# Kernel optimization log

Hardware: AMD Instinct MI355X
Metric: run time of the kernel (lower is better)

Reference implementation:

```python
import jax, jax.numpy as jnp
import numpy as np

D_MODEL = 192
D_STATE = 16
D_CONV = 4
EXPAND = 2
D_INNER = EXPAND * D_MODEL
DT_RANK = (D_MODEL + 15) // 16  # ceil(d_model/16) = 12


def setup_inputs() -> dict:
    key = jax.random.key(0)
    ks = jax.random.split(key, 12)
    B, C, H, W = 16, D_MODEL, 64, 64
    s = lambda n: 0.02
    return {
        "x": jax.random.normal(ks[0], (B, C, H, W), jnp.float32),
        "ln_g": jnp.ones((C,), jnp.float32),
        "ln_b": jnp.zeros((C,), jnp.float32),
        "W_in": jax.random.normal(ks[1], (D_MODEL, 2 * D_INNER), jnp.float32) * s(0),
        "conv_w": jax.random.normal(ks[2], (D_INNER, D_CONV), jnp.float32) * 0.1,
        "conv_b": jnp.zeros((D_INNER,), jnp.float32),
        "W_x": jax.random.normal(ks[3], (D_INNER, DT_RANK + 2 * D_STATE), jnp.float32) * s(0),
        "W_dt": jax.random.normal(ks[4], (DT_RANK, D_INNER), jnp.float32) * 0.1,
        "b_dt": jax.random.uniform(ks[5], (D_INNER,), jnp.float32, -4.0, -1.0),
        "A_log": jnp.log(jnp.broadcast_to(jnp.arange(1, D_STATE + 1, dtype=jnp.float32), (D_INNER, D_STATE))),
        "Dp": jnp.ones((D_INNER,), jnp.float32),
        "W_out": jax.random.normal(ks[6], (D_INNER, D_MODEL), jnp.float32) * s(0),
    }


def _layernorm2d(x, g, b, eps=1e-5):
    # x: (B, C, H, W); normalize over channel dim
    mu = jnp.mean(x, axis=1, keepdims=True)
    var = jnp.var(x, axis=1, keepdims=True)
    xn = (x - mu) * jax.lax.rsqrt(var + eps)
    return xn * g[None, :, None, None] + b[None, :, None, None]


def _mamba(x, W_in, conv_w, conv_b, W_x, W_dt, b_dt, A_log, Dp, W_out):
    # x: (B, L, d_model)
    B, L, _ = x.shape
    xz = x @ W_in                       # (B, L, 2*d_inner)
    xi, z = jnp.split(xz, 2, axis=-1)   # each (B, L, d_inner)

    # causal depthwise conv over L
    xc = jnp.transpose(xi, (0, 2, 1))   # (B, d_inner, L)
    k = conv_w[:, None, :]              # (d_inner, 1, d_conv)
    xc = jax.lax.conv_general_dilated(
        xc, k, window_strides=(1,), padding=[(D_CONV - 1, 0)],
        dimension_numbers=("NCH", "OIH", "NCH"), feature_group_count=D_INNER)
    xc = xc + conv_b[None, :, None]
    u = jax.nn.silu(jnp.transpose(xc, (0, 2, 1)))  # (B, L, d_inner)

    xdbc = u @ W_x                      # (B, L, dt_rank + 2*d_state)
    dt_r, Bm, Cm = jnp.split(xdbc, [DT_RANK, DT_RANK + D_STATE], axis=-1)
    dt = jax.nn.softplus(dt_r @ W_dt + b_dt)  # (B, L, d_inner)
    A = -jnp.exp(A_log)                 # (d_inner, d_state)

    def step(h, inp):
        u_t, dt_t, B_t, C_t = inp       # (B,di), (B,di), (B,ds), (B,ds)
        dA = jnp.exp(dt_t[..., None] * A)              # (B, di, ds)
        dBu = (dt_t * u_t)[..., None] * B_t[:, None, :]  # (B, di, ds)
        h = h * dA + dBu
        y = jnp.einsum("bds,bs->bd", h, C_t)
        return h, y

    h0 = jnp.zeros((B, D_INNER, D_STATE), x.dtype)
    seq = (jnp.moveaxis(u, 1, 0), jnp.moveaxis(dt, 1, 0),
           jnp.moveaxis(Bm, 1, 0), jnp.moveaxis(Cm, 1, 0))
    _, ys = jax.lax.scan(step, h0, seq)
    y = jnp.moveaxis(ys, 0, 1) + u * Dp  # (B, L, d_inner)
    y = y * jax.nn.silu(z)
    return y @ W_out                    # (B, L, d_model)


def reference(x, ln_g, ln_b, W_in, conv_w, conv_b, W_x, W_dt, b_dt, A_log, Dp, W_out):
    b, c, h, w = x.shape
    residual = x
    xn = _layernorm2d(x, ln_g, ln_b)
    seq = jnp.transpose(xn.reshape(b, c, h * w), (0, 2, 1))  # (B, L, C)
    out = _mamba(seq, W_in, conv_w, conv_b, W_x, W_dt, b_dt, A_log, Dp, W_out)
    out = jnp.transpose(out, (0, 2, 1)).reshape(b, c, h, w)
    return out + residual
```

## Files before the change

### kernel.cpp

```cpp
#include <hip/hip_runtime.h>

typedef unsigned short u16;
typedef unsigned int u32;
typedef __attribute__((ext_vector_type(8))) short short8;
typedef __attribute__((ext_vector_type(4))) float f32x4;
typedef __attribute__((ext_vector_type(2))) float f32x2;

#define DEV __device__ __forceinline__

DEV float b2f(u16 u) { union { u32 i; float f; } v; v.i = ((u32)u) << 16; return v.f; }
DEV u16 f2b(float f) {
  union { float f; u32 i; } v; v.f = f;
  u32 r = v.i + 0x7FFFu + ((v.i >> 16) & 1u);
  return (u16)(r >> 16);
}
DEV bool sniff_f32(const void* ln_g) { return ((const u32*)ln_g)[0] == 0x3F800000u; }
DEV float rdv(const void* p, size_t i, bool f32) {
  return f32 ? ((const float*)p)[i] : b2f(((const u16*)p)[i]);
}

__global__ __launch_bounds__(256) void k0_prep(
    const void* __restrict__ W_in, const void* __restrict__ W_out,
    const void* __restrict__ W_x, const void* __restrict__ W_dt,
    const void* __restrict__ b_dt, const void* __restrict__ conv_w,
    const void* __restrict__ conv_b, const void* __restrict__ A_log,
    const void* __restrict__ Dp, const void* __restrict__ ln_g,
    const void* __restrict__ ln_b,
    u16* __restrict__ WinT, u16* __restrict__ WoutT, u16* __restrict__ WbigT,
    float* __restrict__ BdtF, float* __restrict__ convW, float* __restrict__ convB,
    float* __restrict__ AlnF, float* __restrict__ DpF,
    float* __restrict__ lnG, float* __restrict__ lnB) {
  const bool f32 = sniff_f32(ln_g);
  int i = blockIdx.x * 256 + threadIdx.x;
  if (i < 147456) { int n = i / 192, k = i - n * 192; WinT[i] = f2b(rdv(W_in, (size_t)k * 768 + n, f32)); return; }
  i -= 147456;
  if (i < 73728) { int c = i / 384, d = i - c * 384; WoutT[i] = f2b(rdv(W_out, (size_t)d * 192 + c, f32)); return; }
  i -= 73728;
  if (i < 196608) {
    int n = i / 384, k = i - n * 384;
    float v;
    if (n < 384) {
      v = 0.f;
      for (int r = 0; r < 12; ++r)
        v = fmaf(rdv(W_x, (size_t)k * 44 + r, f32), rdv(W_dt, (size_t)r * 384 + n, f32), v);
    } else if (n < 400) {
      v = rdv(W_x, (size_t)k * 44 + 12 + (n - 384), f32);
    } else if (n < 416) {
      v = rdv(W_x, (size_t)k * 44 + 28 + (n - 400), f32);
    } else {
      v = 0.f;
    }
    WbigT[i] = f2b(v);
    return;
  }
  i -= 196608;
  if (i < 384) { BdtF[i] = rdv(b_dt, i, f32); return; }
  i -= 384;
  if (i < 1536) { convW[i] = rdv(conv_w, i, f32); return; }
  i -= 1536;
  if (i < 384) { convB[i] = rdv(conv_b, i, f32); return; }
  i -= 384;
  if (i < 6144) { AlnF[i] = -__expf(rdv(A_log, i, f32)); return; }
  i -= 6144;
  if (i < 384) { DpF[i] = rdv(Dp, i, f32); return; }
  i -= 384;
  if (i < 192) { lnG[i] = rdv(ln_g, i, f32); return; }
  i -= 192;
  if (i < 192) { lnB[i] = rdv(ln_b, i, f32); return; }
}

__global__ __launch_bounds__(192) void k1_ln(
    const void* __restrict__ xg, const void* __restrict__ lng_raw,
    const float* __restrict__ lnG, const float* __restrict__ lnB,
    u16* __restrict__ xn) {
  const bool f32 = sniff_f32(lng_raw);
  const int b = blockIdx.y, l0 = blockIdx.x * 64, t = threadIdx.x;
  __shared__ float xs[192][65];
  __shared__ float rs[3][64], rq[3][64], smu[64], srstd[64];

  for (int i = t; i < 192 * 64; i += 192) {
    int c = i >> 6, l = i & 63;
    xs[c][l] = rdv(xg, ((size_t)(b * 192 + c)) * 4096 + l0 + l, f32);
  }
  __syncthreads();
  const int part = t >> 6, l = t & 63;
  float s = 0.f, q2 = 0.f;
  for (int cc = 0; cc < 64; ++cc) {
    float v = xs[part * 64 + cc][l];
    s += v; q2 = fmaf(v, v, q2);
  }
  rs[part][l] = s; rq[part][l] = q2;
  __syncthreads();
  if (t < 64) {
    float S = rs[0][t] + rs[1][t] + rs[2][t];
    float Q = rq[0][t] + rq[1][t] + rq[2][t];
    float mu = S * (1.0f / 192.0f);
    float var = Q * (1.0f / 192.0f) - mu * mu;
    smu[t] = mu; srstd[t] = rsqrtf(var + 1e-5f);
  }
  __syncthreads();
  const float gv = lnG[t], bv = lnB[t];
  for (int ll = 0; ll < 64; ++ll) {
    float v = (xs[t][ll] - smu[ll]) * srstd[ll];
    xn[((size_t)(b * 4096 + l0 + ll)) * 192 + t] = f2b(fmaf(v, gv, bv));
  }
}

__global__ __launch_bounds__(256) void k2_gemm1(
    const u16* __restrict__ WinT, const u16* __restrict__ xn,
    u16* __restrict__ xz) {
  const int ch0 = blockIdx.x * 128, l0 = blockIdx.y * 128, b = blockIdx.z;
  const int tid = threadIdx.x;
  const int wave = tid >> 6, lane = tid & 63;
  const int wr = wave >> 1, wc = wave & 1;
  const int q = lane >> 4, lm = lane & 15;

  __shared__ __align__(16) u16 As[128][72];
  __shared__ __align__(16) u16 Bs[128][72];

  f32x4 acc[4][4];
#pragma unroll
  for (int i = 0; i < 4; ++i)
#pragma unroll
    for (int j = 0; j < 4; ++j) acc[i][j] = (f32x4){0.f, 0.f, 0.f, 0.f};

  const int r4 = tid >> 3, c8 = (tid & 7) * 8;

  for (int kb = 0; kb < 3; ++kb) {
    const int c0 = kb * 64;
    __syncthreads();
#pragma unroll
    for (int p = 0; p < 4; ++p) {
      int r = p * 32 + r4;
      *(uint4*)&As[r][c8] = *(const uint4*)(WinT + (size_t)(ch0 + r) * 192 + c0 + c8);
      *(uint4*)&Bs[r][c8] = *(const uint4*)(xn + ((size_t)b * 4096 + l0 + r) * 192 + c0 + c8);
    }
    __syncthreads();
#pragma unroll
    for (int ks = 0; ks < 2; ++ks) {
      short8 a[4], bfr[4];
#pragma unroll
      for (int mt = 0; mt < 4; ++mt)
        a[mt] = *(const short8*)&As[wr * 64 + mt * 16 + lm][ks * 32 + q * 8];
#pragma unroll
      for (int nt = 0; nt < 4; ++nt)
        bfr[nt] = *(const short8*)&Bs[wc * 64 + nt * 16 + lm][ks * 32 + q * 8];
#pragma unroll
      for (int mt = 0; mt < 4; ++mt)
#pragma unroll
        for (int nt = 0; nt < 4; ++nt)
          acc[mt][nt] = __builtin_amdgcn_mfma_f32_16x16x32_bf16(a[mt], bfr[nt], acc[mt][nt], 0, 0, 0);
    }
  }
#pragma unroll
  for (int mt = 0; mt < 4; ++mt)
#pragma unroll
    for (int nt = 0; nt < 4; ++nt) {
      int n = l0 + wc * 64 + nt * 16 + lm;
#pragma unroll
      for (int reg = 0; reg < 4; ++reg) {
        int m = ch0 + wr * 64 + mt * 16 + q * 4 + reg;
        xz[((size_t)b * 768 + m) * 4096 + n] = f2b(acc[mt][nt][reg]);
      }
    }
}

__global__ __launch_bounds__(256) void k3_conv(
    u16* __restrict__ xz, const float* __restrict__ convW,
    const float* __restrict__ convB) {
  const int d = blockIdx.x, b = blockIdx.y, t = threadIdx.x;
  u16* row = xz + ((size_t)b * 768 + d) * 4096;
  __shared__ __align__(16) u16 srow[4096];
#pragma unroll
  for (int p = 0; p < 2; ++p)
    *(uint4*)&srow[p * 2048 + t * 8] = *(const uint4*)(row + p * 2048 + t * 8);
  __syncthreads();
  const float w0 = convW[d * 4 + 0], w1 = convW[d * 4 + 1];
  const float w2 = convW[d * 4 + 2], w3 = convW[d * 4 + 3];
  const float cb = convB[d];
  const int l = t * 16;
  u16 o[16];
#pragma unroll
  for (int i = 0; i < 16; ++i) {
    int li = l + i;
    float x0 = (li >= 3) ? b2f(srow[li - 3]) : 0.f;
    float x1 = (li >= 2) ? b2f(srow[li - 2]) : 0.f;
    float x2 = (li >= 1) ? b2f(srow[li - 1]) : 0.f;
    float x3 = b2f(srow[li]);
    float s = w0 * x0 + w1 * x1 + w2 * x2 + w3 * x3 + cb;
    float sig = 1.0f / (1.0f + __expf(-s));
    o[i] = f2b(s * sig);
  }
#pragma unroll
  for (int i = 0; i < 4; ++i) {
    ushort4 st; st.x = o[i * 4 + 0]; st.y = o[i * 4 + 1];
    st.z = o[i * 4 + 2]; st.w = o[i * 4 + 3];
    *(ushort4*)(row + l + i * 4) = st;
  }
}

__global__ __launch_bounds__(256) void k4_mfma(
    const u16* __restrict__ WbigT, const u16* __restrict__ xz,
    const float* __restrict__ BdtF,
    u16* __restrict__ dtb, float* __restrict__ Btl, float* __restrict__ Ctl) {
  const int ch0 = blockIdx.x * 128, l0 = blockIdx.y * 128, b = blockIdx.z;
  const int tid = threadIdx.x;
  const int wave = tid >> 6, lane = tid & 63;
  const int wr = wave >> 1, wc = wave & 1;
  const int q = lane >> 4, lm = lane & 15;

  __shared__ __align__(16) u16 As[128][72];
  __shared__ __align__(16) u16 Bs[128][72];

  f32x4 acc[4][4];
#pragma unroll
  for (int i = 0; i < 4; ++i)
#pragma unroll
    for (int j = 0; j < 4; ++j) acc[i][j] = (f32x4){0.f, 0.f, 0.f, 0.f};

  const int r4 = tid >> 3, c8 = (tid & 7) * 8;
  const int rb = tid >> 5, l4b = (tid & 31) * 4;

  for (int kb = 0; kb < 6; ++kb) {
    const int d0 = kb * 64;
    __syncthreads();
#pragma unroll
    for (int p = 0; p < 4; ++p) {
      int r = p * 32 + r4;
      *(uint4*)&As[r][c8] = *(const uint4*)(WbigT + (size_t)(ch0 + r) * 384 + d0 + c8);
    }
#pragma unroll
    for (int p = 0; p < 8; ++p) {
      int dd = p * 8 + rb;
      ushort4 vv = *(const ushort4*)(xz + ((size_t)b * 768 + d0 + dd) * 4096 + l0 + l4b);
      const int g = dd >> 3, d7 = dd & 7;
      const u16 vals[4] = {vv.x, vv.y, vv.z, vv.w};
#pragma unroll
      for (int i = 0; i < 4; ++i) {
        int l = l4b + i;
        int sc = (((g ^ ((l >> 2) & 7)) << 3) | d7);
        Bs[l][sc] = vals[i];
      }
    }
    __syncthreads();
#pragma unroll
    for (int ks = 0; ks < 2; ++ks) {
      short8 a[4], bfr[4];
#pragma unroll
      for (int mt = 0; mt < 4; ++mt)
        a[mt] = *(const short8*)&As[wr * 64 + mt * 16 + lm][ks * 32 + q * 8];
#pragma unroll
      for (int nt = 0; nt < 4; ++nt) {
        int row = wc * 64 + nt * 16 + lm;
        int g2 = (ks * 4 + q) ^ ((row >> 2) & 7);
        bfr[nt] = *(const short8*)&Bs[row][g2 * 8];
      }
#pragma unroll
      for (int mt = 0; mt < 4; ++mt)
#pragma unroll
        for (int nt = 0; nt < 4; ++nt)
          acc[mt][nt] = __builtin_amdgcn_mfma_f32_16x16x32_bf16(a[mt], bfr[nt], acc[mt][nt], 0, 0, 0);
    }
  }
#pragma unroll
  for (int mt = 0; mt < 4; ++mt) {
    const int tbase = ch0 + wr * 64 + mt * 16;
#pragma unroll
    for (int nt = 0; nt < 4; ++nt) {
      const int l = l0 + wc * 64 + nt * 16 + lm;
      if (tbase < 384) {
#pragma unroll
        for (int reg = 0; reg < 4; ++reg) {
          int m = tbase + q * 4 + reg;
          float v = acc[mt][nt][reg] + BdtF[m];
          float sp = __logf(1.0f + __expf(v));
          dtb[((size_t)b * 384 + m) * 4096 + l] = f2b(sp);
        }
      } else if (tbase == 384) {
        float4 v; v.x = acc[mt][nt][0]; v.y = acc[mt][nt][1];
        v.z = acc[mt][nt][2]; v.w = acc[mt][nt][3];
        *(float4*)(Btl + (((size_t)b * 4096 + l) << 4) + q * 4) = v;
      } else if (tbase == 400) {
        float4 v; v.x = acc[mt][nt][0]; v.y = acc[mt][nt][1];
        v.z = acc[mt][nt][2]; v.w = acc[mt][nt][3];
        *(float4*)(Ctl + (((size_t)b * 4096 + l) << 4) + q * 4) = v;
      }
    }
  }
}

#define NCH 128
#define TCH 32

DEV void build_e8p(float dt, const float* ap, int sbase, bool powok, f32x2* e2) {
  if (powok) {
    float q1 = __expf(-dt);
    float q2 = q1 * q1, q3 = q2 * q1, q4 = q2 * q2;
    float q5 = q4 * q1, q6 = q4 * q2, q7 = q4 * q3, q8 = q4 * q4;
    f32x2 m2; m2.x = sbase ? q8 : 1.0f; m2.y = m2.x;
    f32x2 a0; a0.x = q1; a0.y = q2;
    f32x2 a1; a1.x = q3; a1.y = q4;
    f32x2 a2; a2.x = q5; a2.y = q6;
    f32x2 a3; a3.x = q7; a3.y = q8;
    e2[0] = a0 * m2; e2[1] = a1 * m2; e2[2] = a2 * m2; e2[3] = a3 * m2;
  } else {
#pragma unroll
    for (int k = 0; k < 4; ++k) {
      f32x2 v;
      v.x = __expf(dt * ap[sbase + 2 * k]);
      v.y = __expf(dt * ap[sbase + 2 * k + 1]);
      e2[k] = v;
    }
  }
}

__global__ __launch_bounds__(64) void k5a_part(
    const u16* __restrict__ dtg, const u16* __restrict__ xz,
    const float* __restrict__ Btl, const float* __restrict__ AlnF,
    u16* __restrict__ Sbuf, float* __restrict__ sumdt) {
  const int cx = blockIdx.x, dg0 = blockIdx.y * 32, b = blockIdx.z;
  const int t = threadIdx.x;
  const int sh = t >> 5, dl = t & 31;
  const int sbase = sh * 8;
  const int lc = cx * TCH;
  __shared__ __align__(16) u16 sdt[32][40], su[32][40];
  __shared__ __align__(16) float sB[TCH][16];
#pragma unroll
  for (int i = t; i < 128; i += 64) {
    int r = i >> 2, c8 = (i & 3) * 8;
    *(uint4*)&sdt[r][c8] = *(const uint4*)(dtg + ((size_t)b * 384 + dg0 + r) * 4096 + lc + c8);
    *(uint4*)&su[r][c8] = *(const uint4*)(xz + ((size_t)b * 768 + dg0 + r) * 4096 + lc + c8);
  }
#pragma unroll
  for (int i = t; i < 128; i += 64) {
    int r = i >> 2, c4 = (i & 3) * 4;
    *(float4*)&sB[r][c4] = *(const float4*)(Btl + (((size_t)b * 4096 + lc + r) << 4) + c4);
  }
  __syncthreads();

  const float* ap = AlnF + (dg0 + dl) * 16;
  bool powok = true;
#pragma unroll
  for (int k = 0; k < 8; ++k)
    powok = powok && (fabsf(ap[sbase + k] + (float)(sbase + k + 1)) < 1e-3f * (float)(sbase + k + 1));

  f32x2 S2[4];
#pragma unroll
  for (int k = 0; k < 4; ++k) S2[k] = (f32x2){0.f, 0.f};
  float sdsum = 0.f;

#pragma unroll 1
  for (int l8 = 0; l8 < TCH / 8; ++l8) {
    short8 d8 = *(const short8*)&sdt[dl][l8 * 8];
    short8 u8 = *(const short8*)&su[dl][l8 * 8];
#pragma unroll
    for (int j = 0; j < 8; ++j) {
      float dt = b2f((u16)d8[j]);
      float uu = b2f((u16)u8[j]);
      float dtu = dt * uu;
      sdsum += dt;
      f32x2 e2[4];
      build_e8p(dt, ap, sbase, powok, e2);
      const float* Bp = &sB[l8 * 8 + j][sbase];
      float4 Bv0 = *(const float4*)(Bp);
      float4 Bv1 = *(const float4*)(Bp + 4);
      f32x2 dtu2; dtu2.x = dtu; dtu2.y = dtu;
      f32x2 b0; b0.x = Bv0.x; b0.y = Bv0.y;
      f32x2 b1; b1.x = Bv0.z; b1.y = Bv0.w;
      f32x2 b2; b2.x = Bv1.x; b2.y = Bv1.y;
      f32x2 b3; b3.x = Bv1.z; b3.y = Bv1.w;
      S2[0] = S2[0] * e2[0] + dtu2 * b0;
      S2[1] = S2[1] * e2[1] + dtu2 * b1;
      S2[2] = S2[2] * e2[2] + dtu2 * b2;
      S2[3] = S2[3] * e2[3] + dtu2 * b3;
    }
  }
  const size_t base = (((size_t)b * NCH + cx) * 384 + dg0 + dl) * 16 + sbase;
  u32 w[4];
#pragma unroll
  for (int k = 0; k < 4; ++k)
    w[k] = (u32)f2b(S2[k].x) | ((u32)f2b(S2[k].y) << 16);
  uint4 st0; st0.x = w[0]; st0.y = w[1]; st0.z = w[2]; st0.w = w[3];
  *(uint4*)(Sbuf + base) = st0;
  if (sh == 0)
    sumdt[((size_t)b * NCH + cx) * 384 + dg0 + dl] = sdsum;
}

__global__ __launch_bounds__(256) void k5b_comb(
    u16* __restrict__ Sbuf, const float* __restrict__ sumdt,
    const float* __restrict__ AlnF) {
  const int idx = blockIdx.x * 256 + threadIdx.x;
  const int s = idx & 15;
  const int bd = idx >> 4;
  const int d = bd % 384;
  const float a = AlnF[d * 16 + s];
  const size_t base0 = (size_t)bd * 16 + s;
  const float* sdp = sumdt + bd;
  float h = 0.f;
  float Sv_next = b2f(Sbuf[base0]);
  float sd_next = sdp[0];
  for (int c = 0; c < NCH; ++c) {
    float Sv = Sv_next, sd = sd_next;
    if (c + 1 < NCH) {
      Sv_next = b2f(Sbuf[base0 + (size_t)(c + 1) * 6144]);
      sd_next = sdp[(size_t)(c + 1) * 384];
    }
    Sbuf[base0 + (size_t)c * 6144] = f2b(h);
    h = fmaf(h, __expf(a * sd), Sv);
  }
}

__global__ __launch_bounds__(64) void k5c_scan(
    const u16* __restrict__ dtg, u16* __restrict__ xz,
    const float* __restrict__ Btl, const float* __restrict__ Ctl,
    const u16* __restrict__ Sbuf, const float* __restrict__ AlnF,
    const float* __restrict__ DpF) {
  const int cx = blockIdx.x, dg0 = blockIdx.y * 32, b = blockIdx.z;
  const int t = threadIdx.x;
  const int sh = t >> 5, dl = t & 31;
  const int sbase = sh * 8;
  const int lc = cx * TCH;
  __shared__ __align__(16) u16 sdt[32][40], su[32][40], sz[32][40];
  __shared__ __align__(16) float sB[TCH][16], sC[TCH][16];
#pragma unroll
  for (int i = t; i < 128; i += 64) {
    int r = i >> 2, c8 = (i & 3) * 8;
    *(uint4*)&sdt[r][c8] = *(const uint4*)(dtg + ((size_t)b * 384 + dg0 + r) * 4096 + lc + c8);
    *(uint4*)&su[r][c8] = *(const uint4*)(xz + ((size_t)b * 768 + dg0 + r) * 4096 + lc + c8);
    *(uint4*)&sz[r][c8] = *(const uint4*)(xz + ((size_t)b * 768 + 384 + dg0 + r) * 4096 + lc + c8);
  }
#pragma unroll
  for (int i = t; i < 128; i += 64) {
    int r = i >> 2, c4 = (i & 3) * 4;
    *(float4*)&sB[r][c4] = *(const float4*)(Btl + (((size_t)b * 4096 + lc + r) << 4) + c4);
    *(float4*)&sC[r][c4] = *(const float4*)(Ctl + (((size_t)b * 4096 + lc + r) << 4) + c4);
  }
  __syncthreads();

  const float* ap = AlnF + (dg0 + dl) * 16;
  bool powok = true;
#pragma unroll
  for (int k = 0; k < 8; ++k)
    powok = powok && (fabsf(ap[sbase + k] + (float)(sbase + k + 1)) < 1e-3f * (float)(sbase + k + 1));
  const float Dpl = DpF[dg0 + dl];

  f32x2 h2[4];
  {
    const size_t base = (((size_t)b * NCH + cx) * 384 + dg0 + dl) * 16 + sbase;
    uint4 s0 = *(const uint4*)(Sbuf + base);
    const u32 w[4] = {s0.x, s0.y, s0.z, s0.w};
#pragma unroll
    for (int k = 0; k < 4; ++k) {
      f32x2 v; v.x = b2f((u16)(w[k] & 0xFFFF)); v.y = b2f((u16)(w[k] >> 16));
      h2[k] = v;
    }
  }

  u16* zrow = xz + ((size_t)b * 768 + 384 + dg0 + dl) * 4096;

#pragma unroll 1
  for (int l8 = 0; l8 < TCH / 8; ++l8) {
    short8 d8 = *(const short8*)&sdt[dl][l8 * 8];
    short8 u8 = *(const short8*)&su[dl][l8 * 8];
    short8 z8 = *(const short8*)&sz[dl][l8 * 8];
    float yh[8];
#pragma unroll
    for (int j = 0; j < 8; ++j) {
      float dt = b2f((u16)d8[j]);
      float uu = b2f((u16)u8[j]);
      float dtu = dt * uu;
      f32x2 e2[4];
      build_e8p(dt, ap, sbase, powok, e2);
      const float* Bp = &sB[l8 * 8 + j][sbase];
      const float* Cp = &sC[l8 * 8 + j][sbase];
      float4 Bv0 = *(const float4*)(Bp);
      float4 Bv1 = *(const float4*)(Bp + 4);
      float4 Cv0 = *(const float4*)(Cp);
      float4 Cv1 = *(const float4*)(Cp + 4);
      f32x2 dtu2; dtu2.x = dtu; dtu2.y = dtu;
      f32x2 b0; b0.x = Bv0.x; b0.y = Bv0.y;
      f32x2 b1; b1.x = Bv0.z; b1.y = Bv0.w;
      f32x2 b2; b2.x = Bv1.x; b2.y = Bv1.y;
      f32x2 b3; b3.x = Bv1.z; b3.y = Bv1.w;
      f32x2 c0; c0.x = Cv0.x; c0.y = Cv0.y;
      f32x2 c1; c1.x = Cv0.z; c1.y = Cv0.w;
      f32x2 c2; c2.x = Cv1.x; c2.y = Cv1.y;
      f32x2 c3; c3.x = Cv1.z; c3.y = Cv1.w;
      h2[0] = h2[0] * e2[0] + dtu2 * b0;
      h2[1] = h2[1] * e2[1] + dtu2 * b1;
      h2[2] = h2[2] * e2[2] + dtu2 * b2;
      h2[3] = h2[3] * e2[3] + dtu2 * b3;
      f32x2 y2 = h2[0] * c0;
      y2 = h2[1] * c1 + y2;
      y2 = h2[2] * c2 + y2;
      y2 = h2[3] * c3 + y2;
      yh[j] = y2.x + y2.y;
    }
    u32 ya[4];
#pragma unroll
    for (int j = 0; j < 8; ++j) {
      float yfull = yh[j] + __shfl_xor(yh[j], 32, 64);
      float uu2 = b2f((u16)u8[j]);
      float zz2 = b2f((u16)z8[j]);
      float yf = fmaf(uu2, Dpl, yfull);
      float sig = 1.0f / (1.0f + __expf(-zz2));
      yf *= zz2 * sig;
      u16 yb = f2b(yf);
      if (j & 1) ya[j >> 1] |= ((u32)yb << 16);
      else ya[j >> 1] = (u32)yb;
    }
    if (sh == 0) {
      uint4 st; st.x = ya[0]; st.y = ya[1]; st.z = ya[2]; st.w = ya[3];
      *(uint4*)(zrow + lc + l8 * 8) = st;
    }
  }
}

__global__ __launch_bounds__(256) void k6_gemm2(
    const u16* __restrict__ WoutT, const u16* __restrict__ xz,
    const void* __restrict__ xg, const void* __restrict__ lng_raw,
    void* __restrict__ outg) {
  const bool f32 = sniff_f32(lng_raw);
  const int l0 = blockIdx.x * 128, b = blockIdx.y;
  const int tid = threadIdx.x;
  const int wave = tid >> 6, lane = tid & 63;
  const int wm = wave >> 1, wn = wave & 1;
  const int q = lane >> 4, lm = lane & 15;

  __shared__ __align__(16) u16 As[192][72];
  __shared__ __align__(16) u16 Bs[128][72];

  f32x4 acc[6][4];
#pragma unroll
  for (int i = 0; i < 6; ++i)
#pragma unroll
    for (int j = 0; j < 4; ++j) acc[i][j] = (f32x4){0.f, 0.f, 0.f, 0.f};

  const int ra = tid >> 3, c8 = (tid & 7) * 8;
  const int rb = tid >> 5, l4b = (tid & 31) * 4;

  for (int kb = 0; kb < 6; ++kb) {
    const int d0 = kb * 64;
    __syncthreads();
#pragma unroll
    for (int p = 0; p < 6; ++p) {
      int r = p * 32 + ra;
      *(uint4*)&As[r][c8] = *(const uint4*)(WoutT + (size_t)r * 384 + d0 + c8);
    }
#pragma unroll
    for (int p = 0; p < 8; ++p) {
      int dd = p * 8 + rb;
      ushort4 vv = *(const ushort4*)(xz + ((size_t)b * 768 + 384 + d0 + dd) * 4096 + l0 + l4b);
      const int g = dd >> 3, d7 = dd & 7;
      const u16 vals[4] = {vv.x, vv.y, vv.z, vv.w};
#pragma unroll
      for (int i = 0; i < 4; ++i) {
        int l = l4b + i;
        int sc = (((g ^ ((l >> 2) & 7)) << 3) | d7);
        Bs[l][sc] = vals[i];
      }
    }
    __syncthreads();
#pragma unroll
    for (int ks = 0; ks < 2; ++ks) {
      short8 a[6], bfr[4];
#pragma unroll
      for (int mt = 0; mt < 6; ++mt)
        a[mt] = *(const short8*)&As[wm * 96 + mt * 16 + lm][ks * 32 + q * 8];
#pragma unroll
      for (int nt = 0; nt < 4; ++nt) {
        int row = wn * 64 + nt * 16 + lm;
        int g2 = (ks * 4 + q) ^ ((row >> 2) & 7);
        bfr[nt] = *(const short8*)&Bs[row][g2 * 8];
      }
#pragma unroll
      for (int mt = 0; mt < 6; ++mt)
#pragma unroll
        for (int nt = 0; nt < 4; ++nt)
          acc[mt][nt] = __builtin_amdgcn_mfma_f32_16x16x32_bf16(a[mt], bfr[nt], acc[mt][nt], 0, 0, 0);
    }
  }
  if (f32) {
    float* op = (float*)outg;
    const float* xp = (const float*)xg;
#pragma unroll
    for (int mt = 0; mt < 6; ++mt)
#pragma unroll
      for (int nt = 0; nt < 4; ++nt) {
        int l = l0 + wn * 64 + nt * 16 + lm;
#pragma unroll
        for (int reg = 0; reg < 4; ++reg) {
          int m = wm * 96 + mt * 16 + q * 4 + reg;
          size_t idx = ((size_t)b * 192 + m) * 4096 + l;
          op[idx] = acc[mt][nt][reg] + xp[idx];
        }
      }
  } else {
    u16* op = (u16*)outg;
    const u16* xp = (const u16*)xg;
#pragma unroll
    for (int mt = 0; mt < 6; ++mt)
#pragma unroll
      for (int nt = 0; nt < 4; ++nt) {
        int l = l0 + wn * 64 + nt * 16 + lm;
#pragma unroll
        for (int reg = 0; reg < 4; ++reg) {
          int m = wm * 96 + mt * 16 + q * 4 + reg;
          size_t idx = ((size_t)b * 192 + m) * 4096 + l;
          op[idx] = f2b(acc[mt][nt][reg] + b2f(xp[idx]));
        }
      }
  }
}

extern "C" void kernel_launch(void* const* d_in, const int* in_sizes, int n_in,
                              void* d_out, int out_size, void* d_ws, size_t ws_size,
                              hipStream_t stream) {
  (void)in_sizes; (void)n_in; (void)out_size; (void)ws_size;
  const void* x      = d_in[0];
  const void* ln_g   = d_in[1];
  const void* ln_b   = d_in[2];
  const void* W_in   = d_in[3];
  const void* conv_w = d_in[4];
  const void* conv_b = d_in[5];
  const void* W_x    = d_in[6];
  const void* W_dt   = d_in[7];
  const void* b_dt   = d_in[8];
  const void* A_log  = d_in[9];
  const void* Dp     = d_in[10];
  const void* W_out  = d_in[11];

  char* ws = (char*)d_ws;
  u16*   xz    = (u16*)(ws + 0);
  u16*   xn    = (u16*)(ws + 100663296);
  u16*   dtb   = (u16*)(ws + 100663296);
  float* Btl   = (float*)(ws + 150994944);
  float* Ctl   = (float*)(ws + 155189248);
  u16*   Sbuf  = (u16*)(ws + 159383552);
  float* sumdt = (float*)(ws + 184549376);
  u16*   WinT  = (u16*)(ws + 187695104);
  u16*   WoutT = (u16*)(ws + 187990016);
  u16*   WbigT = (u16*)(ws + 188137472);
  float* BdtF  = (float*)(ws + 188530688);
  float* convW = (float*)(ws + 188532224);
  float* convB = (float*)(ws + 188538368);
  float* AlnF  = (float*)(ws + 188539904);
  float* DpF   = (float*)(ws + 188564480);
  float* lnG   = (float*)(ws + 188566016);
  float* lnB   = (float*)(ws + 188566784);

  k0_prep<<<dim3(1668), dim3(256), 0, stream>>>(
      W_in, W_out, W_x, W_dt, b_dt, conv_w, conv_b, A_log, Dp, ln_g, ln_b,
      WinT, WoutT, WbigT, BdtF, convW, convB, AlnF, DpF, lnG, lnB);
  k1_ln<<<dim3(64, 16), dim3(192), 0, stream>>>(x, ln_g, lnG, lnB, xn);
  k2_gemm1<<<dim3(6, 32, 16), dim3(256), 0, stream>>>(WinT, xn, xz);
  k3_conv<<<dim3(384, 16), dim3(256), 0, stream>>>(xz, convW, convB);
  k4_mfma<<<dim3(4, 32, 16), dim3(256), 0, stream>>>(WbigT, xz, BdtF, dtb, Btl, Ctl);
  k5a_part<<<dim3(NCH, 12, 16), dim3(64), 0, stream>>>(dtb, xz, Btl, AlnF, Sbuf, sumdt);
  k5b_comb<<<dim3(384), dim3(256), 0, stream>>>(Sbuf, sumdt, AlnF);
  k5c_scan<<<dim3(NCH, 12, 16), dim3(64), 0, stream>>>(dtb, xz, Btl, Ctl, Sbuf, AlnF, DpF);
  k6_gemm2<<<dim3(32, 16), dim3(256), 0, stream>>>(WoutT, xz, x, ln_g, (void*)d_out);
}
```

Baseline: 569.5 us.

## Restructure chunked selective scan: larger chunks, 256-thread blocks, register-prefetched row loads

Doubles the scan chunk length and halves the number of chunks. The partial-state and scan kernels now use 256-thread blocks covering 128 channels each, in place of 64-thread blocks. The dt, u and z rows are no longer staged through LDS: each thread reads its own row straight from global memory and prefetches the next 8 elements into registers. The combine kernel's chunk indexing is rewritten to use an explicit per-batch chunk stride, which also corrects the old indexing that was wrong for batches other than the first. The aim is less LDS staging, fewer blocks and less sequential combine work, at the cost of longer serial chunks, lower parallelism and per-lane non-coalesced row loads. The prefetch also reads one vector past the end of each chunk.

```diff
diff --git a/kernel.cpp b/kernel.cpp
--- a/kernel.cpp
+++ b/kernel.cpp
@@ -289,8 +289,8 @@
   }
 }
 
-#define NCH 128
-#define TCH 32
+#define NCH 64
+#define TCH 64
 
 DEV void build_e8p(float dt, const float* ap, int sbase, bool powok, f32x2* e2) {
   if (powok) {
@@ -314,49 +314,50 @@
   }
 }
 
-__global__ __launch_bounds__(64) void k5a_part(
+__global__ __launch_bounds__(256, 4) void k5a_part(
     const u16* __restrict__ dtg, const u16* __restrict__ xz,
     const float* __restrict__ Btl, const float* __restrict__ AlnF,
     u16* __restrict__ Sbuf, float* __restrict__ sumdt) {
-  const int cx = blockIdx.x, dg0 = blockIdx.y * 32, b = blockIdx.z;
+  const int cx = blockIdx.x, b = blockIdx.z;
   const int t = threadIdx.x;
-  const int sh = t >> 5, dl = t & 31;
+  const int wave = t >> 6, lane = t & 63;
+  const int dg0 = blockIdx.y * 128 + wave * 32;
+  const int sh = lane >> 5, dl = lane & 31;
   const int sbase = sh * 8;
   const int lc = cx * TCH;
-  __shared__ __align__(16) u16 sdt[32][40], su[32][40];
   __shared__ __align__(16) float sB[TCH][16];
-#pragma unroll
-  for (int i = t; i < 128; i += 64) {
-    int r = i >> 2, c8 = (i & 3) * 8;
-    *(uint4*)&sdt[r][c8] = *(const uint4*)(dtg + ((size_t)b * 384 + dg0 + r) * 4096 + lc + c8);
-    *(uint4*)&su[r][c8] = *(const uint4*)(xz + ((size_t)b * 768 + dg0 + r) * 4096 + lc + c8);
-  }
-#pragma unroll
-  for (int i = t; i < 128; i += 64) {
-    int r = i >> 2, c4 = (i & 3) * 4;
+  {
+    const int r = t >> 2, c4 = (t & 3) * 4;
     *(float4*)&sB[r][c4] = *(const float4*)(Btl + (((size_t)b * 4096 + lc + r) << 4) + c4);
   }
-  __syncthreads();
-
-  const float* ap = AlnF + (dg0 + dl) * 16;
+  const int d = dg0 + dl;
+  const u16* dtrow = dtg + ((size_t)b * 384 + d) * 4096 + lc;
+  const u16* urow  = xz  + ((size_t)b * 768 + d) * 4096 + lc;
+
+  const float* ap = AlnF + d * 16;
   bool powok = true;
 #pragma unroll
   for (int k = 0; k < 8; ++k)
     powok = powok && (fabsf(ap[sbase + k] + (float)(sbase + k + 1)) < 1e-3f * (float)(sbase + k + 1));
 
+  short8 dcur = *(const short8*)(dtrow);
+  short8 ucur = *(const short8*)(urow);
+
   f32x2 S2[4];
 #pragma unroll
   for (int k = 0; k < 4; ++k) S2[k] = (f32x2){0.f, 0.f};
   float sdsum = 0.f;
 
+  __syncthreads();
+
 #pragma unroll 1
   for (int l8 = 0; l8 < TCH / 8; ++l8) {
-    short8 d8 = *(const short8*)&sdt[dl][l8 * 8];
-    short8 u8 = *(const short8*)&su[dl][l8 * 8];
+    short8 dnxt = *(const short8*)(dtrow + (l8 + 1) * 8);
+    short8 unxt = *(const short8*)(urow + (l8 + 1) * 8);
 #pragma unroll
     for (int j = 0; j < 8; ++j) {
-      float dt = b2f((u16)d8[j]);
-      float uu = b2f((u16)u8[j]);
+      float dt = b2f((u16)dcur[j]);
+      float uu = b2f((u16)ucur[j]);
       float dtu = dt * uu;
       sdsum += dt;
       f32x2 e2[4];
@@ -374,8 +375,9 @@
       S2[2] = S2[2] * e2[2] + dtu2 * b2;
       S2[3] = S2[3] * e2[3] + dtu2 * b3;
     }
-  }
-  const size_t base = (((size_t)b * NCH + cx) * 384 + dg0 + dl) * 16 + sbase;
+    dcur = dnxt; ucur = unxt;
+  }
+  const size_t base = (((size_t)b * NCH + cx) * 384 + d) * 16 + sbase;
   u32 w[4];
 #pragma unroll
   for (int k = 0; k < 4; ++k)
@@ -383,7 +385,7 @@
   uint4 st0; st0.x = w[0]; st0.y = w[1]; st0.z = w[2]; st0.w = w[3];
   *(uint4*)(Sbuf + base) = st0;
   if (sh == 0)
-    sumdt[((size_t)b * NCH + cx) * 384 + dg0 + dl] = sdsum;
+    sumdt[((size_t)b * NCH + cx) * 384 + d] = sdsum;
 }
 
 __global__ __launch_bounds__(256) void k5b_comb(
@@ -392,61 +394,59 @@
   const int idx = blockIdx.x * 256 + threadIdx.x;
   const int s = idx & 15;
   const int bd = idx >> 4;
-  const int d = bd % 384;
+  const int b = bd / 384;
+  const int d = bd - b * 384;
   const float a = AlnF[d * 16 + s];
-  const size_t base0 = (size_t)bd * 16 + s;
-  const float* sdp = sumdt + bd;
+  const size_t cstride = 384 * 16;
+  const size_t base0 = ((size_t)b * NCH) * cstride + (size_t)d * 16 + s;
+  const float* sdp = sumdt + (size_t)b * NCH * 384 + d;
   float h = 0.f;
   float Sv_next = b2f(Sbuf[base0]);
   float sd_next = sdp[0];
   for (int c = 0; c < NCH; ++c) {
     float Sv = Sv_next, sd = sd_next;
     if (c + 1 < NCH) {
-      Sv_next = b2f(Sbuf[base0 + (size_t)(c + 1) * 6144]);
+      Sv_next = b2f(Sbuf[base0 + (size_t)(c + 1) * cstride]);
       sd_next = sdp[(size_t)(c + 1) * 384];
     }
-    Sbuf[base0 + (size_t)c * 6144] = f2b(h);
+    Sbuf[base0 + (size_t)c * cstride] = f2b(h);
     h = fmaf(h, __expf(a * sd), Sv);
   }
 }
 
-__global__ __launch_bounds__(64) void k5c_scan(
+__global__ __launch_bounds__(256, 4) void k5c_scan(
     const u16* __restrict__ dtg, u16* __restrict__ xz,
     const float* __restrict__ Btl, const float* __restrict__ Ctl,
     const u16* __restrict__ Sbuf, const float* __restrict__ AlnF,
     const float* __restrict__ DpF) {
-  const int cx = blockIdx.x, dg0 = blockIdx.y * 32, b = blockIdx.z;
+  const int cx = blockIdx.x, b = blockIdx.z;
   const int t = threadIdx.x;
-  const int sh = t >> 5, dl = t & 31;
+  const int wave = t >> 6, lane = t & 63;
+  const int dg0 = blockIdx.y * 128 + wave * 32;
+  const int sh = lane >> 5, dl = lane & 31;
   const int sbase = sh * 8;
   const int lc = cx * TCH;
-  __shared__ __align__(16) u16 sdt[32][40], su[32][40], sz[32][40];
   __shared__ __align__(16) float sB[TCH][16], sC[TCH][16];
-#pragma unroll
-  for (int i = t; i < 128; i += 64) {
-    int r = i >> 2, c8 = (i & 3) * 8;
-    *(uint4*)&sdt[r][c8] = *(const uint4*)(dtg + ((size_t)b * 384 + dg0 + r) * 4096 + lc + c8);
-    *(uint4*)&su[r][c8] = *(const uint4*)(xz + ((size_t)b * 768 + dg0 + r) * 4096 + lc + c8);
-    *(uint4*)&sz[r][c8] = *(const uint4*)(xz + ((size_t)b * 768 + 384 + dg0 + r) * 4096 + lc + c8);
-  }
-#pragma unroll
-  for (int i = t; i < 128; i += 64) {
-    int r = i >> 2, c4 = (i & 3) * 4;
+  {
+    const int r = t >> 2, c4 = (t & 3) * 4;
     *(float4*)&sB[r][c4] = *(const float4*)(Btl + (((size_t)b * 4096 + lc + r) << 4) + c4);
     *(float4*)&sC[r][c4] = *(const float4*)(Ctl + (((size_t)b * 4096 + lc + r) << 4) + c4);
   }
-  __syncthreads();
-
-  const float* ap = AlnF + (dg0 + dl) * 16;
+  const int d = dg0 + dl;
+  const u16* dtrow = dtg + ((size_t)b * 384 + d) * 4096 + lc;
+  const u16* urow  = xz  + ((size_t)b * 768 + d) * 4096 + lc;
+  u16* zrow = xz + ((size_t)b * 768 + 384 + d) * 4096 + lc;
+
+  const float* ap = AlnF + d * 16;
   bool powok = true;
 #pragma unroll
   for (int k = 0; k < 8; ++k)
     powok = powok && (fabsf(ap[sbase + k] + (float)(sbase + k + 1)) < 1e-3f * (float)(sbase + k + 1));
-  const float Dpl = DpF[dg0 + dl];
+  const float Dpl = DpF[d];
 
   f32x2 h2[4];
   {
-    const size_t base = (((size_t)b * NCH + cx) * 384 + dg0 + dl) * 16 + sbase;
+    const size_t base = (((size_t)b * NCH + cx) * 384 + d) * 16 + sbase;
     uint4 s0 = *(const uint4*)(Sbuf + base);
     const u32 w[4] = {s0.x, s0.y, s0.z, s0.w};
 #pragma unroll
@@ -456,18 +456,22 @@
     }
   }
 
-  u16* zrow = xz + ((size_t)b * 768 + 384 + dg0 + dl) * 4096;
+  short8 dcur = *(const short8*)(dtrow);
+  short8 ucur = *(const short8*)(urow);
+  short8 zcur = *(const short8*)(zrow);
+
+  __syncthreads();
 
 #pragma unroll 1
   for (int l8 = 0; l8 < TCH / 8; ++l8) {
-    short8 d8 = *(const short8*)&sdt[dl][l8 * 8];
-    short8 u8 = *(const short8*)&su[dl][l8 * 8];
-    short8 z8 = *(const short8*)&sz[dl][l8 * 8];
+    short8 dnxt = *(const short8*)(dtrow + (l8 + 1) * 8);
+    short8 unxt = *(const short8*)(urow + (l8 + 1) * 8);
+    short8 znxt = *(const short8*)(zrow + (l8 + 1) * 8);
     float yh[8];
 #pragma unroll
     for (int j = 0; j < 8; ++j) {
-      float dt = b2f((u16)d8[j]);
-      float uu = b2f((u16)u8[j]);
+      float dt = b2f((u16)dcur[j]);
+      float uu = b2f((u16)ucur[j]);
       float dtu = dt * uu;
       f32x2 e2[4];
       build_e8p(dt, ap, sbase, powok, e2);
@@ -500,8 +504,8 @@
 #pragma unroll
     for (int j = 0; j < 8; ++j) {
       float yfull = yh[j] + __shfl_xor(yh[j], 32, 64);
-      float uu2 = b2f((u16)u8[j]);
-      float zz2 = b2f((u16)z8[j]);
+      float uu2 = b2f((u16)ucur[j]);
+      float zz2 = b2f((u16)zcur[j]);
       float yf = fmaf(uu2, Dpl, yfull);
       float sig = 1.0f / (1.0f + __expf(-zz2));
       yf *= zz2 * sig;
@@ -511,8 +515,9 @@
     }
     if (sh == 0) {
       uint4 st; st.x = ya[0]; st.y = ya[1]; st.z = ya[2]; st.w = ya[3];
-      *(uint4*)(zrow + lc + l8 * 8) = st;
-    }
+      *(uint4*)(zrow + l8 * 8) = st;
+    }
+    dcur = dnxt; ucur = unxt; zcur = znxt;
   }
 }
 
@@ -656,8 +661,8 @@
   k2_gemm1<<<dim3(6, 32, 16), dim3(256), 0, stream>>>(WinT, xn, xz);
   k3_conv<<<dim3(384, 16), dim3(256), 0, stream>>>(xz, convW, convB);
   k4_mfma<<<dim3(4, 32, 16), dim3(256), 0, stream>>>(WbigT, xz, BdtF, dtb, Btl, Ctl);
-  k5a_part<<<dim3(NCH, 12, 16), dim3(64), 0, stream>>>(dtb, xz, Btl, AlnF, Sbuf, sumdt);
+  k5a_part<<<dim3(NCH, 3, 16), dim3(256), 0, stream>>>(dtb, xz, Btl, AlnF, Sbuf, sumdt);
   k5b_comb<<<dim3(384), dim3(256), 0, stream>>>(Sbuf, sumdt, AlnF);
-  k5c_scan<<<dim3(NCH, 12, 16), dim3(64), 0, stream>>>(dtb, xz, Btl, Ctl, Sbuf, AlnF, DpF);
+  k5c_scan<<<dim3(NCH, 3, 16), dim3(256), 0, stream>>>(dtb, xz, Btl, Ctl, Sbuf, AlnF, DpF);
   k6_gemm2<<<dim3(32, 16), dim3(256), 0, stream>>>(WoutT, xz, x, ln_g, (void*)d_out);
 }
```

New measurement: 1.724 ms. 3.03x slower.
